# Performance work log

Measured on AMD Instinct MI355X. Metric: run time of the kernel, lower is better.

The kernel has to match this reference:

```python
import jax, jax.numpy as jnp
import numpy as np

HIDDEN = 1024
HEADS = 16
HEAD_DIM = HIDDEN // HEADS
SCALE = 1.0 / (HEAD_DIM ** 0.5)


def setup_inputs() -> dict:
    key = jax.random.key(0)
    k1, k2, k3 = jax.random.split(key, 3)
    B, S = 2, 2048
    x = jax.random.normal(k1, (B, S, HIDDEN), dtype=jnp.float32)
    # torch Linear weights: (out_features, in_features), y = x @ W.T
    qkv_w = jax.random.normal(k2, (3 * HIDDEN, HIDDEN), dtype=jnp.float32) * (HIDDEN ** -0.5)
    out_w = jax.random.normal(k3, (HIDDEN, HIDDEN), dtype=jnp.float32) * (HIDDEN ** -0.5)
    return {"x": x, "qkv_w": qkv_w, "out_w": out_w}


def reference(x, qkv_w, out_w):
    B, S, H = x.shape
    qkv = jnp.einsum('bsh,oh->bso', x, qkv_w)  # [B,S,3H]
    q, k, v = jnp.split(qkv, 3, axis=-1)
    def heads(t):
        return t.reshape(B, S, HEADS, HEAD_DIM).transpose(0, 2, 1, 3)  # [B,nh,S,hd]
    q, k, v = heads(q), heads(k), heads(v)
    scores = jnp.einsum('bhqd,bhkd->bhqk', q, k) * SCALE  # [B,nh,S,S]
    attn = jax.nn.softmax(scores, axis=-1)
    out = jnp.einsum('bhqk,bhkd->bhqd', attn, v)  # [B,nh,S,hd]
    out = out.transpose(0, 2, 1, 3).reshape(B, S, H)
    return jnp.einsum('bsh,oh->bso', out, out_w)
```

## Files before the change

kernel.cpp:

```cpp
#include <hip/hip_runtime.h>
#include <hip/hip_bf16.h>

#define BB 2
#define SS 2048
#define HH 1024
#define NH 16
#define HD 64
#define MM (BB * SS)
#define N_QKV (3 * HH)
#define KK HH

typedef __attribute__((ext_vector_type(8))) short short8;
typedef __attribute__((ext_vector_type(4))) float floatx4;
typedef __attribute__((ext_vector_type(16))) float floatx16;

#define MFMA16(a, b, c) __builtin_amdgcn_mfma_f32_16x16x32_bf16(a, b, c, 0, 0, 0)
#define MFMA32(a, b, c) __builtin_amdgcn_mfma_f32_32x32x16_bf16(a, b, c, 0, 0, 0)

__device__ __forceinline__ unsigned short f2bf(float f) {
  unsigned int u = __builtin_bit_cast(unsigned int, f);
  u += 0x7FFFu + ((u >> 16) & 1u);
  return (unsigned short)(u >> 16);
}

__device__ __forceinline__ float fexp2(float x) {
#if __has_builtin(__builtin_amdgcn_exp2f)
  return __builtin_amdgcn_exp2f(x);
#else
  float r; asm("v_exp_f32 %0, %1" : "=v"(r) : "v"(x)); return r;
#endif
}

__device__ __forceinline__ unsigned int pack2e(float lo, float hi) {
  unsigned int a = __builtin_bit_cast(unsigned int, lo) + 0x8000u;
  unsigned int b = __builtin_bit_cast(unsigned int, hi) + 0x8000u;
  return __builtin_amdgcn_perm(b, a, 0x07060302u);
}

__device__ __forceinline__ unsigned int cvtpk(float lo, float hi) {
  unsigned int r;
  asm("v_cvt_pk_bf16_f32 %0, %1, %2" : "=v"(r) : "v"(lo), "v"(hi));
  return r;
}

__device__ __forceinline__ uint4 cvt8pk(float4 lo, float4 hi) {
  uint4 u;
  u.x = cvtpk(lo.x, lo.y);
  u.y = cvtpk(lo.z, lo.w);
  u.z = cvtpk(hi.x, hi.y);
  u.w = cvtpk(hi.z, hi.w);
  return u;
}

__device__ __forceinline__ void gload_lds16(const void* g, void* l) {
  __builtin_amdgcn_global_load_lds((const __attribute__((address_space(1))) void*)g,
                                   (__attribute__((address_space(3))) void*)l,
                                   16, 0, 0);
}

__global__ __launch_bounds__(256) void cast_all(const float* __restrict__ x,
                                                const float* __restrict__ w1,
                                                const float* __restrict__ w2,
                                                unsigned short* __restrict__ xb,
                                                unsigned short* __restrict__ w1b,
                                                unsigned short* __restrict__ w2b) {
  const int NX = MM * KK / 8;
  const int NW1 = N_QKV * KK / 8;
  int i = blockIdx.x * 256 + threadIdx.x;
  const float* s; unsigned short* d; int o;
  if (i < NX)            { s = x;  d = xb;  o = i; }
  else if (i < NX + NW1) { s = w1; d = w1b; o = i - NX; }
  else                   { s = w2; d = w2b; o = i - (NX + NW1); }
  float4 lo = *(const float4*)(s + (size_t)o * 8);
  float4 hi = *(const float4*)(s + (size_t)o * 8 + 4);
  *(uint4*)(d + (size_t)o * 8) = cvt8pk(lo, hi);
}

__global__ __launch_bounds__(256) void cast_g(const float* __restrict__ s,
                                              unsigned short* __restrict__ d) {
  size_t i = (size_t)blockIdx.x * 256 + threadIdx.x;
  float4 lo = *(const float4*)(s + i * 8);
  float4 hi = *(const float4*)(s + i * 8 + 4);
  *(uint4*)(d + i * 8) = cvt8pk(lo, hi);
}

__global__ __launch_bounds__(256) void gemm_qkv_dma(const unsigned short* __restrict__ Xb,
                                                    const unsigned short* __restrict__ Wb,
                                                    unsigned short* __restrict__ qb,
                                                    unsigned short* __restrict__ kb,
                                                    unsigned short* __restrict__ vtb) {
  __shared__ __attribute__((aligned(16))) unsigned short As[2][128 * 64];
  __shared__ __attribute__((aligned(16))) unsigned short Bs[2][128 * 64];
  const int tid = threadIdx.x;
  const int wave = tid >> 6, lane = tid & 63;
  const int quad = lane >> 4, lc = lane & 15;
  const int wg = (blockIdx.x & 7) * 96 + (blockIdx.x >> 3);
  const int m0 = (wg / 24) * 128, n0 = (wg % 24) * 128;
  const int wm = (wave >> 1) * 64, wn = (wave & 1) * 64;

  floatx4 acc[4][4];
#pragma unroll
  for (int i = 0; i < 4; i++)
#pragma unroll
    for (int j = 0; j < 4; j++) acc[i][j] = (floatx4){0.f, 0.f, 0.f, 0.f};

  const int srow = lane >> 3;
  const int schk = (lane & 7) ^ srow;
  const unsigned short* Ab = Xb + (size_t)(m0 + wave * 8 + srow) * KK + schk * 8;
  const unsigned short* Bb = Wb + (size_t)(n0 + wave * 8 + srow) * KK + schk * 8;

#define STAGEQ(buf, k0)                                                          \
  do {                                                                           \
    _Pragma("unroll")                                                            \
    for (int g = 0; g < 4; g++) {                                                \
      gload_lds16(Ab + (size_t)g * 32 * KK + (k0), &As[buf][(g * 32 + wave * 8) * 64]); \
      gload_lds16(Bb + (size_t)g * 32 * KK + (k0), &Bs[buf][(g * 32 + wave * 8) * 64]); \
    }                                                                            \
  } while (0)

  STAGEQ(0, 0);

  const int NIT = KK / 64;
  for (int it = 0; it < NIT; ++it) {
    const int cb = it & 1;
    if (it + 1 < NIT) {
      STAGEQ(cb ^ 1, (it + 1) * 64);
      asm volatile("s_waitcnt vmcnt(8)" ::: "memory");
    } else {
      asm volatile("s_waitcnt vmcnt(0)" ::: "memory");
    }
    __builtin_amdgcn_s_barrier();
    __builtin_amdgcn_sched_barrier(0);
    __builtin_amdgcn_s_setprio(1);
#pragma unroll
    for (int kk = 0; kk < 2; kk++) {
      short8 af[4], bfr[4];
#pragma unroll
      for (int i = 0; i < 4; i++) {
        const int cs = ((kk * 4 + quad) ^ (lc & 7)) << 3;
        af[i]  = *(const short8*)(&As[cb][(wm + i * 16 + lc) * 64 + cs]);
        bfr[i] = *(const short8*)(&Bs[cb][(wn + i * 16 + lc) * 64 + cs]);
      }
#pragma unroll
      for (int i = 0; i < 4; i++)
#pragma unroll
        for (int j = 0; j < 4; j++) acc[i][j] = MFMA16(af[i], bfr[j], acc[i][j]);
    }
    __builtin_amdgcn_s_setprio(0);
    __builtin_amdgcn_sched_barrier(0);
    __builtin_amdgcn_s_barrier();
  }
#undef STAGEQ

  const float QSCALE = 0.125f * 1.44269504f;
#pragma unroll
  for (int j = 0; j < 4; j++) {
    int n = n0 + wn + j * 16 + lc;
#pragma unroll
    for (int i = 0; i < 4; i++) {
      int mbase = m0 + wm + i * 16 + quad * 4;
      int b = mbase >> 11;
      int s0 = mbase & 2047;
      if (n < HH) {
        int h = n >> 6, d = n & 63;
#pragma unroll
        for (int r = 0; r < 4; r++)
          qb[(((size_t)(b * NH + h) * SS + s0 + r) * HD) + d] = f2bf(acc[i][j][r] * QSCALE);
      } else if (n < 2 * HH) {
        int n2 = n - HH; int h = n2 >> 6, d = n2 & 63;
#pragma unroll
        for (int r = 0; r < 4; r++)
          kb[(((size_t)(b * NH + h) * SS + s0 + r) * HD) + d] = f2bf(acc[i][j][r]);
      } else {
        int n2 = n - 2 * HH; int h = n2 >> 6, d = n2 & 63;
        ushort4 p;
        p.x = f2bf(acc[i][j][0]); p.y = f2bf(acc[i][j][1]);
        p.z = f2bf(acc[i][j][2]); p.w = f2bf(acc[i][j][3]);
        *(ushort4*)(vtb + ((size_t)(b * NH + h) * HD + d) * SS + s0) = p;
      }
    }
  }
}

__global__ __launch_bounds__(256) void gemm_qkv_f32(const unsigned short* __restrict__ Xb,
                                                    const float* __restrict__ Wf,
                                                    unsigned short* __restrict__ qb,
                                                    unsigned short* __restrict__ kb,
                                                    unsigned short* __restrict__ vtb) {
  __shared__ __attribute__((aligned(16))) unsigned short As[128 * 32];
  __shared__ __attribute__((aligned(16))) unsigned short Bs[128 * 32];
  const int tid = threadIdx.x;
  const int wave = tid >> 6, lane = tid & 63;
  const int quad = lane >> 4, lc = lane & 15;
  const int m0 = blockIdx.y * 128, n0 = blockIdx.x * 128;
  const int wm = (wave >> 1) * 64, wn = (wave & 1) * 64;
  const int sr = tid >> 2, sc = (tid & 3) * 8;

  floatx4 acc[4][4];
#pragma unroll
  for (int i = 0; i < 4; i++)
#pragma unroll
    for (int j = 0; j < 4; j++) acc[i][j] = (floatx4){0.f, 0.f, 0.f, 0.f};

  const unsigned short* Axp = Xb + (size_t)(m0 + sr) * KK + sc;
  unsigned short* AsD = As + wave * 512;
  const float* Bg = Wf + (size_t)(n0 + sr) * KK + sc;
  unsigned short* BsW = Bs + wave * 512 + lane * 8;
  float4 b0l = *(const float4*)(Bg),                    b0h = *(const float4*)(Bg + 4);
  float4 b1l = *(const float4*)(Bg + (size_t)64 * KK),  b1h = *(const float4*)(Bg + (size_t)64 * KK + 4);

  for (int it = 0; it < KK / 32; ++it) {
    const int k0 = it * 32;
    __syncthreads();
    gload_lds16(Axp + k0, AsD);
    gload_lds16(Axp + (size_t)64 * KK + k0, AsD + 2048);
    *(uint4*)(BsW) = cvt8pk(b0l, b0h);
    *(uint4*)(BsW + 2048) = cvt8pk(b1l, b1h);
    if (it + 1 < KK / 32) {
      b0l = *(const float4*)(Bg + k0 + 32);                    b0h = *(const float4*)(Bg + k0 + 36);
      b1l = *(const float4*)(Bg + k0 + 32 + (size_t)64 * KK);  b1h = *(const float4*)(Bg + k0 + 36 + (size_t)64 * KK);
    }
    __syncthreads();
    short8 af[4], bfr[4];
#pragma unroll
    for (int i = 0; i < 4; i++) {
      af[i]  = *(const short8*)(As + (wm + i * 16 + lc) * 32 + quad * 8);
      bfr[i] = *(const short8*)(Bs + (wn + i * 16 + lc) * 32 + quad * 8);
    }
#pragma unroll
    for (int i = 0; i < 4; i++)
#pragma unroll
      for (int j = 0; j < 4; j++) acc[i][j] = MFMA16(af[i], bfr[j], acc[i][j]);
  }

  const float QSCALE = 0.125f * 1.44269504f;
#pragma unroll
  for (int j = 0; j < 4; j++) {
    int n = n0 + wn + j * 16 + lc;
#pragma unroll
    for (int i = 0; i < 4; i++) {
      int mbase = m0 + wm + i * 16 + quad * 4;
      int b = mbase >> 11;
      int s0 = mbase & 2047;
      if (n < HH) {
        int h = n >> 6, d = n & 63;
#pragma unroll
        for (int r = 0; r < 4; r++)
          qb[(((size_t)(b * NH + h) * SS + s0 + r) * HD) + d] = f2bf(acc[i][j][r] * QSCALE);
      } else if (n < 2 * HH) {
        int n2 = n - HH; int h = n2 >> 6, d = n2 & 63;
#pragma unroll
        for (int r = 0; r < 4; r++)
          kb[(((size_t)(b * NH + h) * SS + s0 + r) * HD) + d] = f2bf(acc[i][j][r]);
      } else {
        int n2 = n - 2 * HH; int h = n2 >> 6, d = n2 & 63;
        ushort4 p;
        p.x = f2bf(acc[i][j][0]); p.y = f2bf(acc[i][j][1]);
        p.z = f2bf(acc[i][j][2]); p.w = f2bf(acc[i][j][3]);
        *(ushort4*)(vtb + ((size_t)(b * NH + h) * HD + d) * SS + s0) = p;
      }
    }
  }
}

__device__ __forceinline__ int co(int row, int c16) {
  return row * 64 + ((c16 ^ ((row ^ (row >> 3)) & 7)) << 3);
}

__global__ __launch_bounds__(256, 2) void attn_kernel(const unsigned short* __restrict__ qg,
                                                      const unsigned short* __restrict__ kg,
                                                      const unsigned short* __restrict__ vtg,
                                                      unsigned short* __restrict__ og) {
  __shared__ __attribute__((aligned(16))) unsigned short Sall[24576];
  unsigned short* Qs = Sall;

  const int tid = threadIdx.x;
  const int w = tid >> 6, lane = tid & 63;
  const int hl = lane >> 5, c = lane & 31;
  const int q0 = blockIdx.x * 128;
  const int head = blockIdx.y, b = blockIdx.z;

  const unsigned short* qbase = qg + (size_t)(b * NH + head) * SS * HD;
  const unsigned short* kbase = kg + (size_t)(b * NH + head) * SS * HD;
  const unsigned short* vbase = vtg + (size_t)(b * NH + head) * HD * SS;

  {
    int row = tid >> 3, cc = tid & 7;
#pragma unroll
    for (int s = 0; s < 4; s++)
      *(uint4*)(Qs + co(row + 32 * s, cc)) =
          *(const uint4*)(qbase + (size_t)(q0 + row + 32 * s) * HD + cc * 8);
  }

  const int frow = tid >> 3, fc = tid & 7;
  uint4 k0r = *(const uint4*)(kbase + (size_t)frow * HD + fc * 8);
  uint4 k1r = *(const uint4*)(kbase + (size_t)(frow + 32) * HD + fc * 8);
  uint4 v0r = *(const uint4*)(vbase + (size_t)frow * SS + fc * 8);
  uint4 v1r = *(const uint4*)(vbase + (size_t)(frow + 32) * SS + fc * 8);
  {
    unsigned short* K0 = Sall + 8192;
    unsigned short* V0 = Sall + 16384;
    *(uint4*)(K0 + co(frow, fc)) = k0r;
    *(uint4*)(K0 + co(frow + 32, fc)) = k1r;
    *(uint4*)(V0 + co(frow, fc)) = v0r;
    *(uint4*)(V0 + co(frow + 32, fc)) = v1r;
  }
  k0r = *(const uint4*)(kbase + (size_t)(64 + frow) * HD + fc * 8);
  k1r = *(const uint4*)(kbase + (size_t)(96 + frow) * HD + fc * 8);
  v0r = *(const uint4*)(vbase + (size_t)frow * SS + 64 + fc * 8);
  v1r = *(const uint4*)(vbase + (size_t)(frow + 32) * SS + 64 + fc * 8);

  floatx16 oacc0, oacc1, lacc;
#pragma unroll
  for (int i = 0; i < 16; i++) { oacc0[i] = 0.f; oacc1[i] = 0.f; lacc[i] = 0.f; }

  short8 ones;
#pragma unroll
  for (int i = 0; i < 8; i++) ones[i] = (short)0x3F80;

  asm volatile("s_waitcnt lgkmcnt(0)" ::: "memory");
  __builtin_amdgcn_s_barrier();
  __builtin_amdgcn_sched_barrier(0);

  short8 qa[4];
#pragma unroll
  for (int ks = 0; ks < 4; ks++)
    qa[ks] = *(const short8*)(Qs + co(w * 32 + c, ks * 2 + hl));

  for (int kt = 0; kt < SS; kt += 64) {
    const int cur = (kt >> 6) & 1;
    unsigned short* Kc = Sall + 8192 + cur * 4096;
    unsigned short* Vc = Sall + 16384 + cur * 4096;

    if (kt + 64 < SS) {
      unsigned short* Kn = Sall + 8192 + (cur ^ 1) * 4096;
      unsigned short* Vn = Sall + 16384 + (cur ^ 1) * 4096;
      *(uint4*)(Kn + co(frow, fc)) = k0r;
      *(uint4*)(Kn + co(frow + 32, fc)) = k1r;
      *(uint4*)(Vn + co(frow, fc)) = v0r;
      *(uint4*)(Vn + co(frow + 32, fc)) = v1r;
      if (kt + 128 < SS) {
        k0r = *(const uint4*)(kbase + (size_t)(kt + 128 + frow) * HD + fc * 8);
        k1r = *(const uint4*)(kbase + (size_t)(kt + 160 + frow) * HD + fc * 8);
        v0r = *(const uint4*)(vbase + (size_t)frow * SS + kt + 128 + fc * 8);
        v1r = *(const uint4*)(vbase + (size_t)(frow + 32) * SS + kt + 128 + fc * 8);
      }
    }

    floatx16 sacc0, sacc1;
#pragma unroll
    for (int i = 0; i < 16; i++) { sacc0[i] = 0.f; sacc1[i] = 0.f; }
    __builtin_amdgcn_s_setprio(1);
#pragma unroll
    for (int ks = 0; ks < 4; ks++) {
      short8 ka0 = *(const short8*)(Kc + co(c, ks * 2 + hl));
      short8 ka1 = *(const short8*)(Kc + co(32 + c, ks * 2 + hl));
      sacc0 = MFMA32(ka0, qa[ks], sacc0);
      sacc1 = MFMA32(ka1, qa[ks], sacc1);
    }
    __builtin_amdgcn_s_setprio(0);

    short8 pb[4];
#pragma unroll
    for (int kb = 0; kb < 4; kb++) {
      const floatx16& s = (kb < 2) ? sacc0 : sacc1;
      int base = (kb & 1) * 8;
      unsigned int u0 = pack2e(fexp2(s[base + 0]), fexp2(s[base + 1]));
      unsigned int u1 = pack2e(fexp2(s[base + 2]), fexp2(s[base + 3]));
      unsigned int u2 = pack2e(fexp2(s[base + 4]), fexp2(s[base + 5]));
      unsigned int u3 = pack2e(fexp2(s[base + 6]), fexp2(s[base + 7]));
      uint4 u = {u0, u1, u2, u3};
      pb[kb] = __builtin_bit_cast(short8, u);
    }

    __builtin_amdgcn_s_setprio(1);
#pragma unroll
    for (int kb = 0; kb < 4; kb++) {
      uint2 lo0 = *(const uint2*)(Vc + co(c, 2 * kb) + 4 * hl);
      uint2 hi0 = *(const uint2*)(Vc + co(c, 2 * kb + 1) + 4 * hl);
      uint4 a0 = {lo0.x, lo0.y, hi0.x, hi0.y};
      short8 va0 = __builtin_bit_cast(short8, a0);
      uint2 lo1 = *(const uint2*)(Vc + co(32 + c, 2 * kb) + 4 * hl);
      uint2 hi1 = *(const uint2*)(Vc + co(32 + c, 2 * kb + 1) + 4 * hl);
      uint4 a1 = {lo1.x, lo1.y, hi1.x, hi1.y};
      short8 va1 = __builtin_bit_cast(short8, a1);
      oacc0 = MFMA32(va0, pb[kb], oacc0);
      oacc1 = MFMA32(va1, pb[kb], oacc1);
      lacc = MFMA32(ones, pb[kb], lacc);
    }
    __builtin_amdgcn_s_setprio(0);

    asm volatile("s_waitcnt lgkmcnt(0)" ::: "memory");
    __builtin_amdgcn_s_barrier();
    __builtin_amdgcn_sched_barrier(0);
  }

  unsigned short* sc = Sall + w * 2176;
  float inv = 1.0f / lacc[0];
#pragma unroll
  for (int t = 0; t < 8; t++) {
    int d0 = ((2 * t) & 3) + 8 * (t >> 1) + 4 * hl;
    *(unsigned int*)(sc + c * 68 + d0) = pack2e(oacc0[2 * t] * inv, oacc0[2 * t + 1] * inv);
    *(unsigned int*)(sc + c * 68 + 32 + d0) = pack2e(oacc1[2 * t] * inv, oacc1[2 * t + 1] * inv);
  }
  {
    int ql = lane >> 1, hf = lane & 1;
    size_t row = (size_t)(b * SS + q0 + w * 32 + ql);
    unsigned short* dst = og + row * HH + head * 64 + hf * 32;
    const unsigned short* srcp = sc + ql * 68 + hf * 32;
#pragma unroll
    for (int s = 0; s < 4; s++) {
      uint2 a = *(const uint2*)(srcp + s * 8);
      uint2 bq = *(const uint2*)(srcp + s * 8 + 4);
      uint4 v = {a.x, a.y, bq.x, bq.y};
      *(uint4*)(dst + s * 8) = v;
    }
  }
}

__global__ __launch_bounds__(256) void gemm_out_dma(const unsigned short* __restrict__ A,
                                                    const unsigned short* __restrict__ Wb,
                                                    float* __restrict__ C) {
  __shared__ __attribute__((aligned(16))) unsigned short As[2][128 * 64];
  __shared__ __attribute__((aligned(16))) unsigned short Bs[2][64 * 64];
  const int tid = threadIdx.x;
  const int wave = tid >> 6, lane = tid & 63;
  const int quad = lane >> 4, lc = lane & 15;
  const int wg = (blockIdx.x & 7) * 64 + (blockIdx.x >> 3);
  const int m0 = (wg / 16) * 128, n0 = (wg % 16) * 64;
  const int wm = (wave >> 1) * 64, wn = (wave & 1) * 32;

  floatx4 acc[4][2];
#pragma unroll
  for (int i = 0; i < 4; i++)
#pragma unroll
    for (int j = 0; j < 2; j++) acc[i][j] = (floatx4){0.f, 0.f, 0.f, 0.f};

  const int srow = lane >> 3;
  const int schk = (lane & 7) ^ srow;
  const unsigned short* Ab = A  + (size_t)(m0 + wave * 8 + srow) * KK + schk * 8;
  const unsigned short* Bb = Wb + (size_t)(n0 + wave * 8 + srow) * KK + schk * 8;

#define STAGEO(buf, k0)                                                          \
  do {                                                                           \
    _Pragma("unroll")                                                            \
    for (int g = 0; g < 4; g++)                                                  \
      gload_lds16(Ab + (size_t)g * 32 * KK + (k0), &As[buf][(g * 32 + wave * 8) * 64]); \
    _Pragma("unroll")                                                            \
    for (int g = 0; g < 2; g++)                                                  \
      gload_lds16(Bb + (size_t)g * 32 * KK + (k0), &Bs[buf][(g * 32 + wave * 8) * 64]); \
  } while (0)

  STAGEO(0, 0);

  const int NIT = KK / 64;
  for (int it = 0; it < NIT; ++it) {
    const int cb = it & 1;
    if (it + 1 < NIT) {
      STAGEO(cb ^ 1, (it + 1) * 64);
      asm volatile("s_waitcnt vmcnt(6)" ::: "memory");
    } else {
      asm volatile("s_waitcnt vmcnt(0)" ::: "memory");
    }
    __builtin_amdgcn_s_barrier();
    __builtin_amdgcn_sched_barrier(0);
    __builtin_amdgcn_s_setprio(1);
#pragma unroll
    for (int kk = 0; kk < 2; kk++) {
      short8 af[4], bfr[2];
#pragma unroll
      for (int i = 0; i < 4; i++)
        af[i] = *(const short8*)(&As[cb][(wm + i * 16 + lc) * 64 + (((kk * 4 + quad) ^ (lc & 7)) << 3)]);
#pragma unroll
      for (int j = 0; j < 2; j++)
        bfr[j] = *(const short8*)(&Bs[cb][(wn + j * 16 + lc) * 64 + (((kk * 4 + quad) ^ (lc & 7)) << 3)]);
#pragma unroll
      for (int i = 0; i < 4; i++)
#pragma unroll
        for (int j = 0; j < 2; j++) acc[i][j] = MFMA16(af[i], bfr[j], acc[i][j]);
    }
    __builtin_amdgcn_s_setprio(0);
    __builtin_amdgcn_sched_barrier(0);
    __builtin_amdgcn_s_barrier();
  }
#undef STAGEO

#pragma unroll
  for (int i = 0; i < 4; i++)
#pragma unroll
    for (int j = 0; j < 2; j++) {
      int m = m0 + wm + i * 16 + quad * 4;
      int n = n0 + wn + j * 16 + lc;
#pragma unroll
      for (int r = 0; r < 4; r++) C[(size_t)(m + r) * HH + n] = acc[i][j][r];
    }
}

extern "C" void kernel_launch(void* const* d_in, const int* in_sizes, int n_in,
                              void* d_out, int out_size, void* d_ws, size_t ws_size,
                              hipStream_t stream) {
  const float* x = (const float*)d_in[0];
  const float* qkv_w = (const float*)d_in[1];
  const float* out_w = (const float*)d_in[2];
  float* out = (float*)d_out;

  char* ws = (char*)d_ws;
  unsigned short* qb  = (unsigned short*)(ws + 0);
  unsigned short* kb  = (unsigned short*)(ws + 8388608);
  unsigned short* vtb = (unsigned short*)(ws + 16777216);
  unsigned short* xb  = (unsigned short*)(ws + 25165824);
  unsigned short* ao  = xb;

  const bool big = ws_size >= 40ull * 1024 * 1024;
  unsigned short* w1b = big ? (unsigned short*)(ws + 33554432) : nullptr;
  unsigned short* w2b = big ? (unsigned short*)(ws + 39845888) : nullptr;

  if (big) {
    cast_all<<<dim3(4096), dim3(256), 0, stream>>>(x, qkv_w, out_w, xb, w1b, w2b);
    gemm_qkv_dma<<<dim3(768), dim3(256), 0, stream>>>(xb, w1b, qb, kb, vtb);
    attn_kernel<<<dim3(SS / 128, NH, BB), dim3(256), 0, stream>>>(qb, kb, vtb, ao);
    gemm_out_dma<<<dim3(512), dim3(256), 0, stream>>>(ao, w2b, out);
  } else {
    unsigned short* wob = qb;
    cast_g<<<dim3(MM * KK / 2048), dim3(256), 0, stream>>>(x, xb);
    gemm_qkv_f32<<<dim3(N_QKV / 128, MM / 128), dim3(256), 0, stream>>>(xb, qkv_w, qb, kb, vtb);
    attn_kernel<<<dim3(SS / 128, NH, BB), dim3(256), 0, stream>>>(qb, kb, vtb, ao);
    cast_g<<<dim3(HH * KK / 2048), dim3(256), 0, stream>>>(out_w, wob);
    gemm_out_dma<<<dim3(512), dim3(256), 0, stream>>>(ao, wob, out);
  }
}
```

Baseline: 185.3 us.

## Software-pipeline attention loop: overlap QK^T of next tile with PV of previous

```diff
diff --git a/kernel.cpp b/kernel.cpp
--- a/kernel.cpp
+++ b/kernel.cpp
@@ -271,7 +271,7 @@
                                                       const unsigned short* __restrict__ kg,
                                                       const unsigned short* __restrict__ vtg,
                                                       unsigned short* __restrict__ og) {
-  __shared__ __attribute__((aligned(16))) unsigned short Sall[24576];
+  __shared__ __attribute__((aligned(16))) unsigned short Sall[28672];
   unsigned short* Qs = Sall;
 
   const int tid = threadIdx.x;
@@ -293,24 +293,29 @@
   }
 
   const int frow = tid >> 3, fc = tid & 7;
-  uint4 k0r = *(const uint4*)(kbase + (size_t)frow * HD + fc * 8);
-  uint4 k1r = *(const uint4*)(kbase + (size_t)(frow + 32) * HD + fc * 8);
-  uint4 v0r = *(const uint4*)(vbase + (size_t)frow * SS + fc * 8);
-  uint4 v1r = *(const uint4*)(vbase + (size_t)(frow + 32) * SS + fc * 8);
-  {
-    unsigned short* K0 = Sall + 8192;
-    unsigned short* V0 = Sall + 16384;
-    *(uint4*)(K0 + co(frow, fc)) = k0r;
-    *(uint4*)(K0 + co(frow + 32, fc)) = k1r;
-    *(uint4*)(V0 + co(frow, fc)) = v0r;
-    *(uint4*)(V0 + co(frow + 32, fc)) = v1r;
-  }
+  uint4 k0r, k1r, v0r, v1r;
+  k0r = *(const uint4*)(kbase + (size_t)frow * HD + fc * 8);
+  k1r = *(const uint4*)(kbase + (size_t)(frow + 32) * HD + fc * 8);
+  v0r = *(const uint4*)(vbase + (size_t)frow * SS + fc * 8);
+  v1r = *(const uint4*)(vbase + (size_t)(frow + 32) * SS + fc * 8);
+  *(uint4*)(Sall + 8192 + co(frow, fc)) = k0r;
+  *(uint4*)(Sall + 8192 + co(frow + 32, fc)) = k1r;
+  *(uint4*)(Sall + 16384 + co(frow, fc)) = v0r;
+  *(uint4*)(Sall + 16384 + co(frow + 32, fc)) = v1r;
   k0r = *(const uint4*)(kbase + (size_t)(64 + frow) * HD + fc * 8);
   k1r = *(const uint4*)(kbase + (size_t)(96 + frow) * HD + fc * 8);
   v0r = *(const uint4*)(vbase + (size_t)frow * SS + 64 + fc * 8);
   v1r = *(const uint4*)(vbase + (size_t)(frow + 32) * SS + 64 + fc * 8);
-
-  floatx16 oacc0, oacc1, lacc;
+  *(uint4*)(Sall + 8192 + 4096 + co(frow, fc)) = k0r;
+  *(uint4*)(Sall + 8192 + 4096 + co(frow + 32, fc)) = k1r;
+  *(uint4*)(Sall + 16384 + 4096 + co(frow, fc)) = v0r;
+  *(uint4*)(Sall + 16384 + 4096 + co(frow + 32, fc)) = v1r;
+  k0r = *(const uint4*)(kbase + (size_t)(128 + frow) * HD + fc * 8);
+  k1r = *(const uint4*)(kbase + (size_t)(160 + frow) * HD + fc * 8);
+  v0r = *(const uint4*)(vbase + (size_t)frow * SS + 128 + fc * 8);
+  v1r = *(const uint4*)(vbase + (size_t)(frow + 32) * SS + 128 + fc * 8);
+
+  floatx16 oacc0, oacc1, lacc, sA0, sA1, sB0, sB1;
 #pragma unroll
   for (int i = 0; i < 16; i++) { oacc0[i] = 0.f; oacc1[i] = 0.f; lacc[i] = 0.f; }
 
@@ -327,43 +332,96 @@
   for (int ks = 0; ks < 4; ks++)
     qa[ks] = *(const short8*)(Qs + co(w * 32 + c, ks * 2 + hl));
 
-  for (int kt = 0; kt < SS; kt += 64) {
-    const int cur = (kt >> 6) & 1;
-    unsigned short* Kc = Sall + 8192 + cur * 4096;
-    unsigned short* Vc = Sall + 16384 + cur * 4096;
-
-    if (kt + 64 < SS) {
-      unsigned short* Kn = Sall + 8192 + (cur ^ 1) * 4096;
-      unsigned short* Vn = Sall + 16384 + (cur ^ 1) * 4096;
-      *(uint4*)(Kn + co(frow, fc)) = k0r;
-      *(uint4*)(Kn + co(frow + 32, fc)) = k1r;
-      *(uint4*)(Vn + co(frow, fc)) = v0r;
-      *(uint4*)(Vn + co(frow + 32, fc)) = v1r;
-      if (kt + 128 < SS) {
-        k0r = *(const uint4*)(kbase + (size_t)(kt + 128 + frow) * HD + fc * 8);
-        k1r = *(const uint4*)(kbase + (size_t)(kt + 160 + frow) * HD + fc * 8);
-        v0r = *(const uint4*)(vbase + (size_t)frow * SS + kt + 128 + fc * 8);
-        v1r = *(const uint4*)(vbase + (size_t)(frow + 32) * SS + kt + 128 + fc * 8);
-      }
-    }
-
-    floatx16 sacc0, sacc1;
-#pragma unroll
-    for (int i = 0; i < 16; i++) { sacc0[i] = 0.f; sacc1[i] = 0.f; }
-    __builtin_amdgcn_s_setprio(1);
+  {
+#pragma unroll
+    for (int i = 0; i < 16; i++) { sA0[i] = 0.f; sA1[i] = 0.f; }
+    const unsigned short* Kc = Sall + 8192;
 #pragma unroll
     for (int ks = 0; ks < 4; ks++) {
       short8 ka0 = *(const short8*)(Kc + co(c, ks * 2 + hl));
       short8 ka1 = *(const short8*)(Kc + co(32 + c, ks * 2 + hl));
-      sacc0 = MFMA32(ka0, qa[ks], sacc0);
-      sacc1 = MFMA32(ka1, qa[ks], sacc1);
-    }
-    __builtin_amdgcn_s_setprio(0);
-
+      sA0 = MFMA32(ka0, qa[ks], sA0);
+      sA1 = MFMA32(ka1, qa[ks], sA1);
+    }
+  }
+  asm volatile("s_waitcnt lgkmcnt(0)" ::: "memory");
+  __builtin_amdgcn_s_barrier();
+  __builtin_amdgcn_sched_barrier(0);
+
+#define ATTN_STEP(T, SP0, SP1, SC0, SC1)                                        \
+  {                                                                             \
+    const int t_ = (T);                                                         \
+    if (t_ + 1 < SS / 64) {                                                     \
+      unsigned short* Kn = Sall + 8192 + ((t_ + 1) & 1) * 4096;                 \
+      unsigned short* Vn = Sall + 16384 + ((t_ + 1) % 3) * 4096;                \
+      *(uint4*)(Kn + co(frow, fc)) = k0r;                                       \
+      *(uint4*)(Kn + co(frow + 32, fc)) = k1r;                                  \
+      *(uint4*)(Vn + co(frow, fc)) = v0r;                                       \
+      *(uint4*)(Vn + co(frow + 32, fc)) = v1r;                                  \
+      if (t_ + 2 < SS / 64) {                                                   \
+        const int kt2 = (t_ + 2) * 64;                                          \
+        k0r = *(const uint4*)(kbase + (size_t)(kt2 + frow) * HD + fc * 8);      \
+        k1r = *(const uint4*)(kbase + (size_t)(kt2 + 32 + frow) * HD + fc * 8); \
+        v0r = *(const uint4*)(vbase + (size_t)frow * SS + kt2 + fc * 8);        \
+        v1r = *(const uint4*)(vbase + (size_t)(frow + 32) * SS + kt2 + fc * 8); \
+      }                                                                         \
+    }                                                                           \
+    const unsigned short* Kc = Sall + 8192 + (t_ & 1) * 4096;                   \
+    const unsigned short* Vp = Sall + 16384 + ((t_ + 2) % 3) * 4096;            \
+    short8 pb[4];                                                               \
+    _Pragma("unroll")                                                           \
+    for (int kb = 0; kb < 4; kb++) {                                            \
+      const floatx16& s = (kb < 2) ? SP0 : SP1;                                 \
+      int base = (kb & 1) * 8;                                                  \
+      unsigned int u0 = pack2e(fexp2(s[base + 0]), fexp2(s[base + 1]));         \
+      unsigned int u1 = pack2e(fexp2(s[base + 2]), fexp2(s[base + 3]));         \
+      unsigned int u2 = pack2e(fexp2(s[base + 4]), fexp2(s[base + 5]));         \
+      unsigned int u3 = pack2e(fexp2(s[base + 6]), fexp2(s[base + 7]));         \
+      uint4 u = {u0, u1, u2, u3};                                               \
+      pb[kb] = __builtin_bit_cast(short8, u);                                   \
+    }                                                                           \
+    _Pragma("unroll")                                                           \
+    for (int i = 0; i < 16; i++) { SC0[i] = 0.f; SC1[i] = 0.f; }                \
+    __builtin_amdgcn_s_setprio(1);                                              \
+    _Pragma("unroll")                                                           \
+    for (int ks = 0; ks < 4; ks++) {                                            \
+      short8 ka0 = *(const short8*)(Kc + co(c, ks * 2 + hl));                   \
+      short8 ka1 = *(const short8*)(Kc + co(32 + c, ks * 2 + hl));              \
+      SC0 = MFMA32(ka0, qa[ks], SC0);                                           \
+      SC1 = MFMA32(ka1, qa[ks], SC1);                                           \
+    }                                                                           \
+    _Pragma("unroll")                                                           \
+    for (int kb = 0; kb < 4; kb++) {                                            \
+      uint2 lo0 = *(const uint2*)(Vp + co(c, 2 * kb) + 4 * hl);                 \
+      uint2 hi0 = *(const uint2*)(Vp + co(c, 2 * kb + 1) + 4 * hl);             \
+      uint4 a0 = {lo0.x, lo0.y, hi0.x, hi0.y};                                  \
+      short8 va0 = __builtin_bit_cast(short8, a0);                              \
+      uint2 lo1 = *(const uint2*)(Vp + co(32 + c, 2 * kb) + 4 * hl);            \
+      uint2 hi1 = *(const uint2*)(Vp + co(32 + c, 2 * kb + 1) + 4 * hl);        \
+      uint4 a1 = {lo1.x, lo1.y, hi1.x, hi1.y};                                  \
+      short8 va1 = __builtin_bit_cast(short8, a1);                              \
+      oacc0 = MFMA32(va0, pb[kb], oacc0);                                       \
+      oacc1 = MFMA32(va1, pb[kb], oacc1);                                       \
+      lacc = MFMA32(ones, pb[kb], lacc);                                        \
+    }                                                                           \
+    __builtin_amdgcn_s_setprio(0);                                              \
+    asm volatile("s_waitcnt lgkmcnt(0)" ::: "memory");                          \
+    __builtin_amdgcn_s_barrier();                                               \
+    __builtin_amdgcn_sched_barrier(0);                                          \
+  }
+
+  for (int tt = 1; tt + 1 < SS / 64; tt += 2) {
+    ATTN_STEP(tt, sA0, sA1, sB0, sB1);
+    ATTN_STEP(tt + 1, sB0, sB1, sA0, sA1);
+  }
+  ATTN_STEP(SS / 64 - 1, sA0, sA1, sB0, sB1);
+
+  {
+    const unsigned short* Vp = Sall + 16384 + ((SS / 64 - 1) % 3) * 4096;
     short8 pb[4];
 #pragma unroll
     for (int kb = 0; kb < 4; kb++) {
-      const floatx16& s = (kb < 2) ? sacc0 : sacc1;
+      const floatx16& s = (kb < 2) ? sB0 : sB1;
       int base = (kb & 1) * 8;
       unsigned int u0 = pack2e(fexp2(s[base + 0]), fexp2(s[base + 1]));
       unsigned int u1 = pack2e(fexp2(s[base + 2]), fexp2(s[base + 3]));
@@ -372,28 +430,23 @@
       uint4 u = {u0, u1, u2, u3};
       pb[kb] = __builtin_bit_cast(short8, u);
     }
-
-    __builtin_amdgcn_s_setprio(1);
 #pragma unroll
     for (int kb = 0; kb < 4; kb++) {
-      uint2 lo0 = *(const uint2*)(Vc + co(c, 2 * kb) + 4 * hl);
-      uint2 hi0 = *(const uint2*)(Vc + co(c, 2 * kb + 1) + 4 * hl);
+      uint2 lo0 = *(const uint2*)(Vp + co(c, 2 * kb) + 4 * hl);
+      uint2 hi0 = *(const uint2*)(Vp + co(c, 2 * kb + 1) + 4 * hl);
       uint4 a0 = {lo0.x, lo0.y, hi0.x, hi0.y};
       short8 va0 = __builtin_bit_cast(short8, a0);
-      uint2 lo1 = *(const uint2*)(Vc + co(32 + c, 2 * kb) + 4 * hl);
-      uint2 hi1 = *(const uint2*)(Vc + co(32 + c, 2 * kb + 1) + 4 * hl);
+      uint2 lo1 = *(const uint2*)(Vp + co(32 + c, 2 * kb) + 4 * hl);
+      uint2 hi1 = *(const uint2*)(Vp + co(32 + c, 2 * kb + 1) + 4 * hl);
       uint4 a1 = {lo1.x, lo1.y, hi1.x, hi1.y};
       short8 va1 = __builtin_bit_cast(short8, a1);
       oacc0 = MFMA32(va0, pb[kb], oacc0);
       oacc1 = MFMA32(va1, pb[kb], oacc1);
       lacc = MFMA32(ones, pb[kb], lacc);
     }
-    __builtin_amdgcn_s_setprio(0);
-
-    asm volatile("s_waitcnt lgkmcnt(0)" ::: "memory");
-    __builtin_amdgcn_s_barrier();
-    __builtin_amdgcn_sched_barrier(0);
-  }
+  }
+  asm volatile("s_waitcnt lgkmcnt(0)" ::: "memory");
+  __builtin_amdgcn_s_barrier();
 
   unsigned short* sc = Sall + w * 2176;
   float inv = 1.0f / lacc[0];
@@ -417,6 +470,7 @@
     }
   }
 }
+#undef ATTN_STEP
 
 __global__ __launch_bounds__(256) void gemm_out_dma(const unsigned short* __restrict__ A,
                                                     const unsigned short* __restrict__ Wb,
```

After: 186.2 us. About the same (+0.4%).
